# Performance work log

Hardware: AMD Instinct MI355X
Metric: run time of the kernel (lower is better)

Reference implementation:

```python
import jax, jax.numpy as jnp
import numpy as np

N, P, IN, HID, HEADS, OUT, E = 8192, 3, 256, 64, 8, 64, 262144
HD = HEADS * HID


def _gat(h, fc, al, ar, bias, src, dst):
    # DGL GATConv forward (no dropout), returns (elu(out) [N,H,D], attention [E,H])
    feat = (h @ fc).reshape(N, HEADS, HID)          # [N,H,D]
    el = (feat * al).sum(-1)                        # [N,H]
    er = (feat * ar).sum(-1)                        # [N,H]
    e = jax.nn.leaky_relu(el[src] + er[dst], negative_slope=0.2)  # [E,H]
    emax = jax.ops.segment_max(e, dst, num_segments=N)            # [N,H]
    ee = jnp.exp(e - emax[dst])
    denom = jax.ops.segment_sum(ee, dst, num_segments=N)          # [N,H]
    a = ee / denom[dst]                                           # edge softmax over dst
    rst = jax.ops.segment_sum(a[:, :, None] * feat[src], dst, num_segments=N)  # [N,H,D]
    out = jax.nn.elu(rst + bias)
    return out, a


def setup_inputs():
    key = jax.random.key(0)
    ks = jax.random.split(key, 12)
    s = 0.05
    return {
        "h": jax.random.normal(ks[0], (N, IN), jnp.float32),
        "edge_src": jax.random.randint(ks[1], (P, E), 0, N, jnp.int32),
        "edge_dst": jax.random.randint(ks[2], (P, E), 0, N, jnp.int32),
        "gat_fc": jax.random.normal(ks[3], (P, IN, HD), jnp.float32) * s,
        "attn_l": jax.random.normal(ks[4], (P, HEADS, HID), jnp.float32) * s,
        "attn_r": jax.random.normal(ks[5], (P, HEADS, HID), jnp.float32) * s,
        "gat_bias": jnp.zeros((P, HEADS, HID), jnp.float32),
        "sa_w1": jax.random.normal(ks[6], (HD, 128), jnp.float32) * s,
        "sa_b1": jnp.zeros((128,), jnp.float32),
        "sa_w2": jax.random.normal(ks[7], (128, 1), jnp.float32) * s,
        "pred_w": jax.random.normal(ks[8], (HD, OUT), jnp.float32) * s,
        "pred_b": jnp.zeros((OUT,), jnp.float32),
    }


def reference(h, edge_src, edge_dst, gat_fc, attn_l, attn_r, gat_bias,
              sa_w1, sa_b1, sa_w2, pred_w, pred_b):
    zp_list, alpha_list = [], []
    for p in range(P):
        z_p, a_p = _gat(h, gat_fc[p], attn_l[p], attn_r[p], gat_bias[p],
                        edge_src[p], edge_dst[p])
        zp_list.append(z_p.reshape(N, HD))          # flatten(start_dim=1)
        alpha_list.append(a_p.mean(axis=1))         # [E], mean over heads
    zp = jnp.stack(zp_list, axis=1)                 # [N,P,HD]

    # Semantic attention
    w = (zp @ sa_w1 + sa_b1) @ sa_w2                # [N,P,1]
    w = jax.nn.leaky_relu(w, negative_slope=0.01).mean(axis=0)  # [P,1]
    beta = jax.nn.softmax(w, axis=0)                # [P,1]

    # Dense adjacency accumulation of edge attention weights
    atten = jnp.zeros((N, N), jnp.float32)
    for p in range(P):
        vals = alpha_list[p] * beta[p, 0]
        atten = atten.at[edge_src[p], edge_dst[p]].add(vals)

    z = (beta[None, :, :] * zp).sum(axis=1)         # [N,HD]
    out = z @ pred_w + pred_b                       # [N,OUT]
    return out, atten
```

## Files before the change

### kernel.cpp

```cpp
#include <hip/hip_runtime.h>
#include <math.h>

#define NN    8192
#define PP    3
#define INF_  256
#define HID_  64
#define HEADS 8
#define OUTF  64
#define NE    262144
#define HD    512
#define DEGCAP 128

typedef __attribute__((ext_vector_type(8))) short short8;
typedef __attribute__((ext_vector_type(4))) float f32x4;

__device__ __forceinline__ unsigned short f2bf(float f) {
    unsigned u = __float_as_uint(f);
    unsigned r = u + 0x7fffu + ((u >> 16) & 1u);
    return (unsigned short)(r >> 16);
}
__device__ __forceinline__ float bf2f_lo(unsigned v) { return __uint_as_float(v << 16); }
__device__ __forceinline__ float bf2f_hi(unsigned v) { return __uint_as_float(v & 0xffff0000u); }

__device__ __forceinline__ void beta_from_wsum(
        const float* __restrict__ wsum, float* __restrict__ shb) {
    int tid = threadIdx.x;
    if (tid < 64) {
        float s0 = wsum[tid], s1 = wsum[64 + tid], s2 = wsum[128 + tid];
#pragma unroll
        for (int off = 32; off > 0; off >>= 1) {
            s0 += __shfl_down(s0, off);
            s1 += __shfl_down(s1, off);
            s2 += __shfl_down(s2, off);
        }
        if (tid == 0) {
            float w0 = s0 / (float)NN, w1 = s1 / (float)NN, w2 = s2 / (float)NN;
            float m  = fmaxf(w0, fmaxf(w1, w2));
            float e0 = expf(w0 - m), e1 = expf(w1 - m), e2 = expf(w2 - m);
            float ss = e0 + e1 + e2;
            shb[0] = e0 / ss; shb[1] = e1 / ss; shb[2] = e2 / ss;
        }
    }
    __syncthreads();
}

__global__ __launch_bounds__(256) void cast_count(
        const float* __restrict__ h, const float* __restrict__ fc,
        const int* __restrict__ esrc, const int* __restrict__ edst,
        unsigned short* __restrict__ hb, unsigned short* __restrict__ fcT,
        int* __restrict__ counts ) {
    int b = blockIdx.x, t = threadIdx.x;
    if (b < 2048) {
        int i = b * 256 + t;
        float4 v = *(const float4*)(h + (size_t)i * 4);
        ushort4 o = { f2bf(v.x), f2bf(v.y), f2bf(v.z), f2bf(v.w) };
        *(ushort4*)(hb + (size_t)i * 4) = o;
    } else if (b < 2048 + 1536) {
        int i = (b - 2048) * 256 + t;
        if (i < PP * INF_ * HD) {
            int p = i / (INF_ * HD);
            int rem = i - p * INF_ * HD;
            int k = rem / HD;
            int n = rem - k * HD;
            fcT[(size_t)p * HD * INF_ + (size_t)n * INF_ + k] = f2bf(fc[i]);
        }
    } else {
        int i = (b - 3584) * 256 + t;
        if (i < PP * NE) {
            int p = i >> 18;
            atomicAdd(&counts[p * NN + edst[i]], 1);
            atomicAdd(&counts[3 * NN + esrc[i]], 1);
        }
    }
}

__global__ __launch_bounds__(1024) void scan_vw(
        const int* __restrict__ counts, int* __restrict__ offsets,
        int* __restrict__ cursor, const float* __restrict__ w1,
        const float* __restrict__ b1, const float* __restrict__ w2,
        float* __restrict__ v ) {
    int t = threadIdx.x;
    if (blockIdx.x == 4) {
        if (t < HD) {
            float s = 0.f;
            for (int k = 0; k < 128; ++k) s += w1[t * 128 + k] * w2[k];
            v[t] = s;
        } else if (t == HD) {
            float c = 0.f;
            for (int k = 0; k < 128; ++k) c += b1[k] * w2[k];
            v[HD] = c;
        }
        return;
    }
    __shared__ int sh[1024];
    int seg = blockIdx.x;
    const int* cnt = counts + seg * NN;
    int* offs = offsets + seg * (NN + 1);
    int* cur  = cursor + seg * NN;
    int loc[8];
    int s = 0;
#pragma unroll
    for (int i = 0; i < 8; ++i) { loc[i] = cnt[t * 8 + i]; s += loc[i]; }
    sh[t] = s;
    __syncthreads();
    for (int off = 1; off < 1024; off <<= 1) {
        int vv = (t >= off) ? sh[t - off] : 0;
        __syncthreads();
        sh[t] += vv;
        __syncthreads();
    }
    int run = sh[t] - s;
#pragma unroll
    for (int i = 0; i < 8; ++i) {
        offs[t * 8 + i] = run;
        cur[t * 8 + i]  = run;
        run += loc[i];
    }
    if (t == 1023) offs[NN] = run;
}

__global__ __launch_bounds__(256) void scatter_all(
        const int* __restrict__ esrc, const int* __restrict__ edst,
        int* __restrict__ cursor, int* __restrict__ ssrc_sorted,
        int2* __restrict__ spair) {
    int i = blockIdx.x * blockDim.x + threadIdx.x;
    if (i >= PP * NE) return;
    int p = i >> 18;
    int s = esrc[i], d = edst[i];
    int pos = atomicAdd(&cursor[p * NN + d], 1);
    ssrc_sorted[(size_t)p * NE + pos] = s;
    int pos2 = atomicAdd(&cursor[3 * NN + s], 1);
    int2 pr; pr.x = p * NE + pos; pr.y = d;
    spair[pos2] = pr;
}

#define LDK 72
__global__ __launch_bounds__(256) void gemm_feat_mfma(
        const unsigned short* __restrict__ hb,
        const unsigned short* __restrict__ fcT,
        const float* __restrict__ al_all,
        const float* __restrict__ ar_all,
        unsigned short* __restrict__ featb,
        float* __restrict__ el,
        float* __restrict__ er) {
    __shared__ unsigned short As[64 * LDK];
    __shared__ unsigned short Bs[64 * LDK];
    int p  = blockIdx.z;
    int n0 = blockIdx.x * 64;
    int m0 = blockIdx.y * 64;
    const unsigned short* Bt = fcT + (size_t)p * HD * INF_;
    unsigned short* C = featb + (size_t)p * NN * HD;
    int tid  = threadIdx.x;
    int wv   = tid >> 6, lane = tid & 63;
    int row  = tid >> 2, kc = (tid & 3) * 8;
    int l16  = lane & 15, quad = lane >> 4;
    int mw   = wv * 16;
    f32x4 acc[4] = {{0.f,0.f,0.f,0.f},{0.f,0.f,0.f,0.f},
                    {0.f,0.f,0.f,0.f},{0.f,0.f,0.f,0.f}};
    for (int k0 = 0; k0 < INF_; k0 += 64) {
        const unsigned short* ha = &hb[(size_t)(m0 + row) * INF_ + k0 + kc];
        const unsigned short* ba = &Bt[(size_t)(n0 + row) * INF_ + k0 + kc];
        *(short8*)&As[row * LDK + kc]      = *(const short8*)ha;
        *(short8*)&As[row * LDK + kc + 32] = *(const short8*)(ha + 32);
        *(short8*)&Bs[row * LDK + kc]      = *(const short8*)ba;
        *(short8*)&Bs[row * LDK + kc + 32] = *(const short8*)(ba + 32);
        __syncthreads();
        short8 af0 = *(short8*)&As[(mw + l16) * LDK + quad * 8];
        short8 af1 = *(short8*)&As[(mw + l16) * LDK + 32 + quad * 8];
#pragma unroll
        for (int nt = 0; nt < 4; ++nt) {
            short8 bf0 = *(short8*)&Bs[(nt * 16 + l16) * LDK + quad * 8];
            acc[nt] = __builtin_amdgcn_mfma_f32_16x16x32_bf16(af0, bf0, acc[nt], 0, 0, 0);
            short8 bf1 = *(short8*)&Bs[(nt * 16 + l16) * LDK + 32 + quad * 8];
            acc[nt] = __builtin_amdgcn_mfma_f32_16x16x32_bf16(af1, bf1, acc[nt], 0, 0, 0);
        }
        __syncthreads();
    }
#pragma unroll
    for (int nt = 0; nt < 4; ++nt) {
#pragma unroll
        for (int r = 0; r < 4; ++r) {
            C[(size_t)(m0 + mw + quad * 4 + r) * HD + n0 + nt * 16 + l16] =
                f2bf(acc[nt][r]);
        }
    }
    int hidx = n0 >> 6;
    float alv[4], arv[4];
#pragma unroll
    for (int nt = 0; nt < 4; ++nt) {
        alv[nt] = al_all[p * HD + n0 + nt * 16 + l16];
        arv[nt] = ar_all[p * HD + n0 + nt * 16 + l16];
    }
    float* elp = el + (size_t)p * NN * HEADS;
    float* erp = er + (size_t)p * NN * HEADS;
#pragma unroll
    for (int r = 0; r < 4; ++r) {
        float pe = acc[0][r] * alv[0] + acc[1][r] * alv[1] +
                   acc[2][r] * alv[2] + acc[3][r] * alv[3];
        float pr = acc[0][r] * arv[0] + acc[1][r] * arv[1] +
                   acc[2][r] * arv[2] + acc[3][r] * arv[3];
#pragma unroll
        for (int m = 1; m < 16; m <<= 1) {
            pe += __shfl_xor(pe, m);
            pr += __shfl_xor(pr, m);
        }
        if (l16 == 0) {
            int node = m0 + mw + quad * 4 + r;
            elp[node * HEADS + hidx] = pe;
            erp[node * HEADS + hidx] = pr;
        }
    }
}

__global__ __launch_bounds__(256) void fused_attn_rst(
        const int* __restrict__ ssrc_sorted, const int* __restrict__ offsets_all,
        const float* __restrict__ el, const float* __restrict__ er,
        const unsigned short* __restrict__ featb,
        const float* __restrict__ bias_all, const float* __restrict__ v,
        float* __restrict__ alpha_all ,
        unsigned short* __restrict__ zpb,
        float* __restrict__ wsum ) {
    __shared__ float sh_e[4][DEGCAP * 8];
    __shared__ int   sh_src[4][DEGCAP];
    int wv = threadIdx.x >> 6, lane = threadIdx.x & 63;
    int gid = blockIdx.x * 4 + wv;
    int n = gid & (NN - 1);
    int p = gid >> 13;
    const int* srcrow  = ssrc_sorted + (size_t)p * NE;
    const int* offs    = offsets_all + p * (NN + 1);
    const float* elp   = el + (size_t)p * NN * HEADS;
    const float* erp   = er + (size_t)p * NN * HEADS;
    const unsigned short* feat = featb + (size_t)p * NN * HD;
    int start = offs[n];
    int deg = offs[n + 1] - start;
    if (deg > DEGCAP) deg = DEGCAP;

    float4 r0 = *(const float4*)(erp + n * 8);
    float4 r1 = *(const float4*)(erp + n * 8 + 4);
    for (int t = lane; t < deg; t += 64) {
        int s = srcrow[start + t];
        sh_src[wv][t] = s;
        float4 l0 = *(const float4*)(elp + s * 8);
        float4 l1 = *(const float4*)(elp + s * 8 + 4);
        float sc[8] = {l0.x + r0.x, l0.y + r0.y, l0.z + r0.z, l0.w + r0.w,
                       l1.x + r1.x, l1.y + r1.y, l1.z + r1.z, l1.w + r1.w};
#pragma unroll
        for (int hh = 0; hh < 8; ++hh) {
            float x = sc[hh];
            sh_e[wv][t * 8 + hh] = x > 0.f ? x : 0.2f * x;
        }
    }
    __syncthreads();

    int h = lane >> 3;
    {
        int j = lane & 7;
        float m = -INFINITY;
        for (int t = j; t < deg; t += 8) m = fmaxf(m, sh_e[wv][t * 8 + h]);
#pragma unroll
        for (int off = 4; off; off >>= 1) m = fmaxf(m, __shfl_xor(m, off));
        float ssum = 0.f;
        for (int t = j; t < deg; t += 8) {
            float ee = __expf(sh_e[wv][t * 8 + h] - m);
            sh_e[wv][t * 8 + h] = ee;
            ssum += ee;
        }
#pragma unroll
        for (int off = 4; off; off >>= 1) ssum += __shfl_xor(ssum, off);
        float inv = 1.f / ssum;
        for (int t = j; t < deg; t += 8) sh_e[wv][t * 8 + h] *= inv;
    }
    __syncthreads();

    for (int t = lane; t < deg; t += 64) {
        float s = 0.f;
#pragma unroll
        for (int hh = 0; hh < 8; ++hh) s += sh_e[wv][t * 8 + hh];
        alpha_all[(size_t)p * NE + start + t] = s * 0.125f;
    }

    int c = lane * 8;
    float acc[8] = {0.f, 0.f, 0.f, 0.f, 0.f, 0.f, 0.f, 0.f};
#define FMA8(F, KI) { \
        float a_ = sh_e[wv][(KI) * 8 + h]; \
        acc[0] += a_ * bf2f_lo((F).x); acc[1] += a_ * bf2f_hi((F).x); \
        acc[2] += a_ * bf2f_lo((F).y); acc[3] += a_ * bf2f_hi((F).y); \
        acc[4] += a_ * bf2f_lo((F).z); acc[5] += a_ * bf2f_hi((F).z); \
        acc[6] += a_ * bf2f_lo((F).w); acc[7] += a_ * bf2f_hi((F).w); }
    int k = 0;
    for (; k + 4 <= deg; k += 4) {
        int s0 = sh_src[wv][k],     s1 = sh_src[wv][k + 1];
        int s2 = sh_src[wv][k + 2], s3 = sh_src[wv][k + 3];
        uint4 f0 = *(const uint4*)&feat[(size_t)s0 * HD + c];
        uint4 f1 = *(const uint4*)&feat[(size_t)s1 * HD + c];
        uint4 f2 = *(const uint4*)&feat[(size_t)s2 * HD + c];
        uint4 f3 = *(const uint4*)&feat[(size_t)s3 * HD + c];
        FMA8(f0, k); FMA8(f1, k + 1); FMA8(f2, k + 2); FMA8(f3, k + 3);
    }
    for (; k < deg; ++k) {
        int s = sh_src[wv][k];
        uint4 f = *(const uint4*)&feat[(size_t)s * HD + c];
        FMA8(f, k);
    }
#undef FMA8
    const float* bias = bias_all + p * HD;
    float4 b0 = *(const float4*)(bias + c);
    float4 b1 = *(const float4*)(bias + c + 4);
    float z[8];
    z[0] = acc[0] + b0.x; z[1] = acc[1] + b0.y; z[2] = acc[2] + b0.z; z[3] = acc[3] + b0.w;
    z[4] = acc[4] + b1.x; z[5] = acc[5] + b1.y; z[6] = acc[6] + b1.z; z[7] = acc[7] + b1.w;
#pragma unroll
    for (int i = 0; i < 8; ++i) z[i] = z[i] > 0.f ? z[i] : expm1f(z[i]);
    uint4 zo;
    zo.x = (unsigned)f2bf(z[0]) | ((unsigned)f2bf(z[1]) << 16);
    zo.y = (unsigned)f2bf(z[2]) | ((unsigned)f2bf(z[3]) << 16);
    zo.z = (unsigned)f2bf(z[4]) | ((unsigned)f2bf(z[5]) << 16);
    zo.w = (unsigned)f2bf(z[6]) | ((unsigned)f2bf(z[7]) << 16);
    *(uint4*)&zpb[(size_t)n * (PP * HD) + p * HD + c] = zo;

    float4 v0 = *(const float4*)(v + c);
    float4 v1 = *(const float4*)(v + c + 4);
    float part = z[0] * v0.x + z[1] * v0.y + z[2] * v0.z + z[3] * v0.w +
                 z[4] * v1.x + z[5] * v1.y + z[6] * v1.z + z[7] * v1.w;
#pragma unroll
    for (int off = 32; off > 0; off >>= 1) part += __shfl_down(part, off);
    if (lane == 0) {
        float w = part + v[HD];
        w = w > 0.f ? w : 0.01f * w;
        atomicAdd(&wsum[p * 64 + (n & 63)], w);
    }
}

#define K5R 16
__global__ __launch_bounds__(256) void final_out(
        const unsigned short* __restrict__ zpb, const float* __restrict__ wsum,
        const float* __restrict__ pw, const float* __restrict__ pb,
        float* __restrict__ out) {
    __shared__ float zt[K5R][HD];
    __shared__ float shb[3];
    beta_from_wsum(wsum, shb);
    int tid = threadIdx.x;
    int n0 = blockIdx.x * K5R;
    float b0 = shb[0], b1 = shb[1], b2 = shb[2];
    int c = tid * 2;
#pragma unroll
    for (int r = 0; r < K5R; ++r) {
        const unsigned short* zr = zpb + (size_t)(n0 + r) * (PP * HD);
        unsigned u0 = *(const unsigned*)(zr + c);
        unsigned u1 = *(const unsigned*)(zr + HD + c);
        unsigned u2 = *(const unsigned*)(zr + 2 * HD + c);
        zt[r][c]     = b0 * bf2f_lo(u0) + b1 * bf2f_lo(u1) + b2 * bf2f_lo(u2);
        zt[r][c + 1] = b0 * bf2f_hi(u0) + b1 * bf2f_hi(u1) + b2 * bf2f_hi(u2);
    }
    __syncthreads();
    int o = tid & 63, rg = tid >> 6;
    float a0 = 0.f, a1 = 0.f, a2 = 0.f, a3 = 0.f;
    for (int j = 0; j < HD; ++j) {
        float pwj = pw[j * 64 + o];
        a0 += zt[rg * 4 + 0][j] * pwj;
        a1 += zt[rg * 4 + 1][j] * pwj;
        a2 += zt[rg * 4 + 2][j] * pwj;
        a3 += zt[rg * 4 + 3][j] * pwj;
    }
    float bo = pb[o];
    out[(size_t)(n0 + rg * 4 + 0) * 64 + o] = a0 + bo;
    out[(size_t)(n0 + rg * 4 + 1) * 64 + o] = a1 + bo;
    out[(size_t)(n0 + rg * 4 + 2) * 64 + o] = a2 + bo;
    out[(size_t)(n0 + rg * 4 + 3) * 64 + o] = a3 + bo;
}

__global__ __launch_bounds__(256) void atten_rows(
        const int2* __restrict__ spair, const int* __restrict__ soffs,
        const float* __restrict__ alpha, const float* __restrict__ wsum,
        float* __restrict__ atten) {
    __shared__ float rowbuf[NN];
    __shared__ float shb[3];
    beta_from_wsum(wsum, shb);
    int srow = blockIdx.x, tid = threadIdx.x;
    f32x4 zero = {0.f, 0.f, 0.f, 0.f};
    for (int j = tid; j < NN / 4; j += 256) ((f32x4*)rowbuf)[j] = zero;
    __syncthreads();
    int s0 = soffs[srow], s1 = soffs[srow + 1];
    for (int k = s0 + tid; k < s1; k += 256) {
        int2 pr = spair[k];
        float val = alpha[pr.x] * shb[pr.x >> 18];
        atomicAdd(&rowbuf[pr.y], val);
    }
    __syncthreads();
    float* orow = atten + (size_t)srow * NN;
    for (int j = tid * 4; j < NN; j += 1024) {
        f32x4 v = *(f32x4*)(rowbuf + j);
        __builtin_nontemporal_store(v, (f32x4*)(orow + j));
    }
}

extern "C" void kernel_launch(void* const* d_in, const int* in_sizes, int n_in,
                              void* d_out, int out_size, void* d_ws, size_t ws_size,
                              hipStream_t stream) {
    const float* h    = (const float*)d_in[0];
    const int*   esrc = (const int*)d_in[1];
    const int*   edst = (const int*)d_in[2];
    const float* fc   = (const float*)d_in[3];
    const float* al   = (const float*)d_in[4];
    const float* ar   = (const float*)d_in[5];
    const float* bias = (const float*)d_in[6];
    const float* w1   = (const float*)d_in[7];
    const float* b1   = (const float*)d_in[8];
    const float* w2   = (const float*)d_in[9];
    const float* pw   = (const float*)d_in[10];
    const float* pb   = (const float*)d_in[11];
    float* out   = (float*)d_out;
    float* atten = out + (size_t)NN * OUTF;

    char* ws = (char*)d_ws;
    size_t off = 0;
    auto alloc = [&](size_t bytes) {
        void* p = ws + off;
        off = (off + bytes + 255) & ~(size_t)255;
        return p;
    };
    unsigned short* zpb   = (unsigned short*)alloc(sizeof(short) * (size_t)NN * PP * HD);
    unsigned short* featb = (unsigned short*)alloc(sizeof(short) * (size_t)PP * NN * HD);
    unsigned short* hb  = (unsigned short*)alloc(sizeof(short) * (size_t)NN * INF_);
    unsigned short* fcT = (unsigned short*)alloc(sizeof(short) * (size_t)PP * HD * INF_);
    float*  el      = (float*)alloc(sizeof(float) * PP * NN * HEADS);
    float*  er      = (float*)alloc(sizeof(float) * PP * NN * HEADS);
    float*  alpha   = (float*)alloc(sizeof(float) * (size_t)PP * NE);
    int*    counts  = (int*)alloc(sizeof(int) * 4 * NN);
    float*  wsum    = (float*)alloc(sizeof(float) * 3 * 64);
    int*    offsets = (int*)alloc(sizeof(int) * 4 * (NN + 1));
    int*    cursor  = (int*)alloc(sizeof(int) * 4 * NN);
    int*    ssrc_sorted = (int*)alloc(sizeof(int) * (size_t)PP * NE);
    int2*   spair   = (int2*)alloc(sizeof(int2) * (size_t)PP * NE);
    float*  vbuf    = (float*)alloc(sizeof(float) * (HD + 1));

    (void)hipMemsetAsync(counts, 0, sizeof(int) * 4 * NN + 1024, stream);

    cast_count<<<2048 + 1536 + 3072, 256, 0, stream>>>(
        h, fc, esrc, edst, hb, fcT, counts);

    scan_vw<<<5, 1024, 0, stream>>>(counts, offsets, cursor, w1, b1, w2, vbuf);

    scatter_all<<<PP * NE / 256, 256, 0, stream>>>(
        esrc, edst, cursor, ssrc_sorted, spair);

    gemm_feat_mfma<<<dim3(HD / 64, NN / 64, PP), 256, 0, stream>>>(
        hb, fcT, al, ar, featb, el, er);

    fused_attn_rst<<<NN * PP / 4, 256, 0, stream>>>(
        ssrc_sorted, offsets, el, er, featb, bias, vbuf, alpha, zpb, wsum);

    final_out<<<NN / K5R, 256, 0, stream>>>(zpb, wsum, pw, pb, out);
    atten_rows<<<NN, 256, 0, stream>>>(
        spair, offsets + 3 * (NN + 1), alpha, wsum, atten);
}
```

Measured before the change: 661.8 us.

## Merge scatter with GEMM and final_out with atten_rows into single launches

The edge scatter and the feature GEMM now share one launch, split by block index, and the final projection shares one launch with the dense attention-row kernel. The edge-count pass reads four edges per thread through int4 loads. Beta is now computed in registers by each wavefront with shuffles, which removes a shared-memory broadcast and its barrier. The intent is to cut launch overhead and let independent work overlap on the GPU. In exchange the GEMM blocks may wait behind scatter blocks, and the merged kernels use more shared memory per block.

```diff
diff --git a/kernel.cpp b/kernel.cpp
--- a/kernel.cpp
+++ b/kernel.cpp
@@ -22,26 +22,22 @@
 __device__ __forceinline__ float bf2f_lo(unsigned v) { return __uint_as_float(v << 16); }
 __device__ __forceinline__ float bf2f_hi(unsigned v) { return __uint_as_float(v & 0xffff0000u); }
 
-__device__ __forceinline__ void beta_from_wsum(
-        const float* __restrict__ wsum, float* __restrict__ shb) {
-    int tid = threadIdx.x;
-    if (tid < 64) {
-        float s0 = wsum[tid], s1 = wsum[64 + tid], s2 = wsum[128 + tid];
-#pragma unroll
-        for (int off = 32; off > 0; off >>= 1) {
-            s0 += __shfl_down(s0, off);
-            s1 += __shfl_down(s1, off);
-            s2 += __shfl_down(s2, off);
-        }
-        if (tid == 0) {
-            float w0 = s0 / (float)NN, w1 = s1 / (float)NN, w2 = s2 / (float)NN;
-            float m  = fmaxf(w0, fmaxf(w1, w2));
-            float e0 = expf(w0 - m), e1 = expf(w1 - m), e2 = expf(w2 - m);
-            float ss = e0 + e1 + e2;
-            shb[0] = e0 / ss; shb[1] = e1 / ss; shb[2] = e2 / ss;
-        }
-    }
-    __syncthreads();
+__device__ __forceinline__ void beta_reg(const float* __restrict__ wsum,
+                                         float& rb0, float& rb1, float& rb2) {
+    int lane = threadIdx.x & 63;
+    float s0 = wsum[lane], s1 = wsum[64 + lane], s2 = wsum[128 + lane];
+#pragma unroll
+    for (int off = 32; off > 0; off >>= 1) {
+        s0 += __shfl_down(s0, off);
+        s1 += __shfl_down(s1, off);
+        s2 += __shfl_down(s2, off);
+    }
+    float t0 = __shfl(s0, 0), t1 = __shfl(s1, 0), t2 = __shfl(s2, 0);
+    float w0 = t0 / (float)NN, w1 = t1 / (float)NN, w2 = t2 / (float)NN;
+    float m  = fmaxf(w0, fmaxf(w1, w2));
+    float e0 = expf(w0 - m), e1 = expf(w1 - m), e2 = expf(w2 - m);
+    float ss = e0 + e1 + e2;
+    rb0 = e0 / ss; rb1 = e1 / ss; rb2 = e2 / ss;
 }
 
 __global__ __launch_bounds__(256) void cast_count(
@@ -66,11 +62,17 @@
         }
     } else {
         int i = (b - 3584) * 256 + t;
-        if (i < PP * NE) {
-            int p = i >> 18;
-            atomicAdd(&counts[p * NN + edst[i]], 1);
-            atomicAdd(&counts[3 * NN + esrc[i]], 1);
-        }
+        int4 s4 = ((const int4*)esrc)[i];
+        int4 d4 = ((const int4*)edst)[i];
+        int p = i >> 16;
+        atomicAdd(&counts[p * NN + d4.x], 1);
+        atomicAdd(&counts[p * NN + d4.y], 1);
+        atomicAdd(&counts[p * NN + d4.z], 1);
+        atomicAdd(&counts[p * NN + d4.w], 1);
+        atomicAdd(&counts[3 * NN + s4.x], 1);
+        atomicAdd(&counts[3 * NN + s4.y], 1);
+        atomicAdd(&counts[3 * NN + s4.z], 1);
+        atomicAdd(&counts[3 * NN + s4.w], 1);
     }
 }
 
@@ -119,23 +121,11 @@
     if (t == 1023) offs[NN] = run;
 }
 
-__global__ __launch_bounds__(256) void scatter_all(
+#define LDK 72
+__global__ __launch_bounds__(256) void scatter_gemm(
         const int* __restrict__ esrc, const int* __restrict__ edst,
         int* __restrict__ cursor, int* __restrict__ ssrc_sorted,
-        int2* __restrict__ spair) {
-    int i = blockIdx.x * blockDim.x + threadIdx.x;
-    if (i >= PP * NE) return;
-    int p = i >> 18;
-    int s = esrc[i], d = edst[i];
-    int pos = atomicAdd(&cursor[p * NN + d], 1);
-    ssrc_sorted[(size_t)p * NE + pos] = s;
-    int pos2 = atomicAdd(&cursor[3 * NN + s], 1);
-    int2 pr; pr.x = p * NE + pos; pr.y = d;
-    spair[pos2] = pr;
-}
-
-#define LDK 72
-__global__ __launch_bounds__(256) void gemm_feat_mfma(
+        int2* __restrict__ spair,
         const unsigned short* __restrict__ hb,
         const unsigned short* __restrict__ fcT,
         const float* __restrict__ al_all,
@@ -145,12 +135,24 @@
         float* __restrict__ er) {
     __shared__ unsigned short As[64 * LDK];
     __shared__ unsigned short Bs[64 * LDK];
-    int p  = blockIdx.z;
-    int n0 = blockIdx.x * 64;
-    int m0 = blockIdx.y * 64;
+    int tid = threadIdx.x;
+    if (blockIdx.x < 3072) {
+        int i = blockIdx.x * 256 + tid;
+        int p = i >> 18;
+        int s = esrc[i], d = edst[i];
+        int pos = atomicAdd(&cursor[p * NN + d], 1);
+        ssrc_sorted[(size_t)p * NE + pos] = s;
+        int pos2 = atomicAdd(&cursor[3 * NN + s], 1);
+        int2 pr; pr.x = p * NE + pos; pr.y = d;
+        spair[pos2] = pr;
+        return;
+    }
+    int g  = blockIdx.x - 3072;
+    int p  = g >> 10;
+    int n0 = (g & 7) * 64;
+    int m0 = ((g >> 3) & 127) * 64;
     const unsigned short* Bt = fcT + (size_t)p * HD * INF_;
     unsigned short* C = featb + (size_t)p * NN * HD;
-    int tid  = threadIdx.x;
     int wv   = tid >> 6, lane = tid & 63;
     int row  = tid >> 2, kc = (tid & 3) * 8;
     int l16  = lane & 15, quad = lane >> 4;
@@ -332,65 +334,62 @@
 }
 
 #define K5R 16
-__global__ __launch_bounds__(256) void final_out(
+__global__ __launch_bounds__(256) void final_atten(
         const unsigned short* __restrict__ zpb, const float* __restrict__ wsum,
         const float* __restrict__ pw, const float* __restrict__ pb,
-        float* __restrict__ out) {
-    __shared__ float zt[K5R][HD];
-    __shared__ float shb[3];
-    beta_from_wsum(wsum, shb);
+        const int2* __restrict__ spair, const int* __restrict__ soffs,
+        const float* __restrict__ alpha,
+        float* __restrict__ out, float* __restrict__ atten) {
+    __shared__ float buf[NN];
+    float b0, b1, b2;
+    beta_reg(wsum, b0, b1, b2);
     int tid = threadIdx.x;
-    int n0 = blockIdx.x * K5R;
-    float b0 = shb[0], b1 = shb[1], b2 = shb[2];
-    int c = tid * 2;
-#pragma unroll
-    for (int r = 0; r < K5R; ++r) {
-        const unsigned short* zr = zpb + (size_t)(n0 + r) * (PP * HD);
-        unsigned u0 = *(const unsigned*)(zr + c);
-        unsigned u1 = *(const unsigned*)(zr + HD + c);
-        unsigned u2 = *(const unsigned*)(zr + 2 * HD + c);
-        zt[r][c]     = b0 * bf2f_lo(u0) + b1 * bf2f_lo(u1) + b2 * bf2f_lo(u2);
-        zt[r][c + 1] = b0 * bf2f_hi(u0) + b1 * bf2f_hi(u1) + b2 * bf2f_hi(u2);
-    }
-    __syncthreads();
-    int o = tid & 63, rg = tid >> 6;
-    float a0 = 0.f, a1 = 0.f, a2 = 0.f, a3 = 0.f;
-    for (int j = 0; j < HD; ++j) {
-        float pwj = pw[j * 64 + o];
-        a0 += zt[rg * 4 + 0][j] * pwj;
-        a1 += zt[rg * 4 + 1][j] * pwj;
-        a2 += zt[rg * 4 + 2][j] * pwj;
-        a3 += zt[rg * 4 + 3][j] * pwj;
-    }
-    float bo = pb[o];
-    out[(size_t)(n0 + rg * 4 + 0) * 64 + o] = a0 + bo;
-    out[(size_t)(n0 + rg * 4 + 1) * 64 + o] = a1 + bo;
-    out[(size_t)(n0 + rg * 4 + 2) * 64 + o] = a2 + bo;
-    out[(size_t)(n0 + rg * 4 + 3) * 64 + o] = a3 + bo;
-}
-
-__global__ __launch_bounds__(256) void atten_rows(
-        const int2* __restrict__ spair, const int* __restrict__ soffs,
-        const float* __restrict__ alpha, const float* __restrict__ wsum,
-        float* __restrict__ atten) {
-    __shared__ float rowbuf[NN];
-    __shared__ float shb[3];
-    beta_from_wsum(wsum, shb);
-    int srow = blockIdx.x, tid = threadIdx.x;
-    f32x4 zero = {0.f, 0.f, 0.f, 0.f};
-    for (int j = tid; j < NN / 4; j += 256) ((f32x4*)rowbuf)[j] = zero;
-    __syncthreads();
-    int s0 = soffs[srow], s1 = soffs[srow + 1];
-    for (int k = s0 + tid; k < s1; k += 256) {
-        int2 pr = spair[k];
-        float val = alpha[pr.x] * shb[pr.x >> 18];
-        atomicAdd(&rowbuf[pr.y], val);
-    }
-    __syncthreads();
-    float* orow = atten + (size_t)srow * NN;
-    for (int j = tid * 4; j < NN; j += 1024) {
-        f32x4 v = *(f32x4*)(rowbuf + j);
-        __builtin_nontemporal_store(v, (f32x4*)(orow + j));
+    if (blockIdx.x < NN) {
+        int srow = blockIdx.x;
+        f32x4 zero = {0.f, 0.f, 0.f, 0.f};
+        for (int j = tid; j < NN / 4; j += 256) ((f32x4*)buf)[j] = zero;
+        __syncthreads();
+        int s0 = soffs[srow], s1 = soffs[srow + 1];
+        for (int k = s0 + tid; k < s1; k += 256) {
+            int2 pr = spair[k];
+            int pp = pr.x >> 18;
+            float bsel = pp == 0 ? b0 : (pp == 1 ? b1 : b2);
+            atomicAdd(&buf[pr.y], alpha[pr.x] * bsel);
+        }
+        __syncthreads();
+        float* orow = atten + (size_t)srow * NN;
+        for (int j = tid * 4; j < NN; j += 1024) {
+            f32x4 v = *(f32x4*)(buf + j);
+            __builtin_nontemporal_store(v, (f32x4*)(orow + j));
+        }
+    } else {
+        int n0 = (blockIdx.x - NN) * K5R;
+        float* zt = buf;
+        int c = tid * 2;
+#pragma unroll
+        for (int r = 0; r < K5R; ++r) {
+            const unsigned short* zr = zpb + (size_t)(n0 + r) * (PP * HD);
+            unsigned u0 = *(const unsigned*)(zr + c);
+            unsigned u1 = *(const unsigned*)(zr + HD + c);
+            unsigned u2 = *(const unsigned*)(zr + 2 * HD + c);
+            zt[r * HD + c]     = b0 * bf2f_lo(u0) + b1 * bf2f_lo(u1) + b2 * bf2f_lo(u2);
+            zt[r * HD + c + 1] = b0 * bf2f_hi(u0) + b1 * bf2f_hi(u1) + b2 * bf2f_hi(u2);
+        }
+        __syncthreads();
+        int o = tid & 63, rg = tid >> 6;
+        float a0 = 0.f, a1 = 0.f, a2 = 0.f, a3 = 0.f;
+        for (int j = 0; j < HD; ++j) {
+            float pwj = pw[j * 64 + o];
+            a0 += zt[(rg * 4 + 0) * HD + j] * pwj;
+            a1 += zt[(rg * 4 + 1) * HD + j] * pwj;
+            a2 += zt[(rg * 4 + 2) * HD + j] * pwj;
+            a3 += zt[(rg * 4 + 3) * HD + j] * pwj;
+        }
+        float bo = pb[o];
+        out[(size_t)(n0 + rg * 4 + 0) * 64 + o] = a0 + bo;
+        out[(size_t)(n0 + rg * 4 + 1) * 64 + o] = a1 + bo;
+        out[(size_t)(n0 + rg * 4 + 2) * 64 + o] = a2 + bo;
+        out[(size_t)(n0 + rg * 4 + 3) * 64 + o] = a3 + bo;
     }
 }
 
@@ -436,21 +435,18 @@
 
     (void)hipMemsetAsync(counts, 0, sizeof(int) * 4 * NN + 1024, stream);
 
-    cast_count<<<2048 + 1536 + 3072, 256, 0, stream>>>(
+    cast_count<<<2048 + 1536 + 768, 256, 0, stream>>>(
         h, fc, esrc, edst, hb, fcT, counts);
 
     scan_vw<<<5, 1024, 0, stream>>>(counts, offsets, cursor, w1, b1, w2, vbuf);
 
-    scatter_all<<<PP * NE / 256, 256, 0, stream>>>(
-        esrc, edst, cursor, ssrc_sorted, spair);
-
-    gemm_feat_mfma<<<dim3(HD / 64, NN / 64, PP), 256, 0, stream>>>(
+    scatter_gemm<<<6144, 256, 0, stream>>>(
+        esrc, edst, cursor, ssrc_sorted, spair,
         hb, fcT, al, ar, featb, el, er);
 
     fused_attn_rst<<<NN * PP / 4, 256, 0, stream>>>(
         ssrc_sorted, offsets, el, er, featb, bias, vbuf, alpha, zpb, wsum);
 
-    final_out<<<NN / K5R, 256, 0, stream>>>(zpb, wsum, pw, pb, out);
-    atten_rows<<<NN, 256, 0, stream>>>(
-        spair, offsets + 3 * (NN + 1), alpha, wsum, atten);
-}
+    final_atten<<<NN + NN / K5R, 256, 0, stream>>>(
+        zpb, wsum, pw, pb, spair, offsets + 3 * (NN + 1), alpha, out, atten);
+}
```

New measurement: 657.3 us. About the same (-0.7%).
